# Kernel tuning notes

Hardware: AMD Instinct MI355X
Metric: run time of the kernel (lower is better)

## Reference

```python
import jax, jax.numpy as jnp
import numpy as np

# dims
B, T = 2, 256
E = 512            # n_embd
G = 8              # n_groups
GD = E // G        # group_dim == head_dim == 64
L = 8              # n_layer
N = L * G          # n_nodes == 64
V = 50257          # vocab
S = 8              # n_steps


def _rms(x):
    eps = jnp.asarray(jnp.finfo(x.dtype).eps, x.dtype)
    return x * jax.lax.rsqrt(jnp.mean(x * x, axis=-1, keepdims=True) + eps)


def _rope(x, cos, sin):
    # x: (B,T,N,GD); cos/sin: (T, GD//2)
    d = x.shape[-1] // 2
    x1, x2 = x[..., :d], x[..., d:]
    c = cos[None, :, None, :]
    s = sin[None, :, None, :]
    return jnp.concatenate([x1 * c + x2 * s, -x1 * s + x2 * c], axis=-1)


def setup_inputs() -> dict:
    key = jax.random.key(0)
    ks = jax.random.split(key, 9)
    idx = jax.random.randint(ks[0], (B, T), 0, V, dtype=jnp.int32)
    wte = 0.02 * jax.random.normal(ks[1], (V, E), jnp.float32)
    # adapters: identity block at group slice (per init_weights) + small noise
    ad = np.zeros((N, GD, E), np.float32)
    for i in range(N):
        g = i % G
        ad[i, :, g * GD:(g + 1) * GD] = np.eye(GD, dtype=np.float32)
    adapters = jnp.asarray(ad) + 0.005 * jax.random.normal(ks[2], (N, GD, E), jnp.float32)
    qkv_w = 0.005 * jax.random.normal(ks[3], (N, 3 * GD, GD), jnp.float32)
    attn_proj = 0.005 * jax.random.normal(ks[4], (N, GD, GD), jnp.float32)
    mlp_fc = 0.005 * jax.random.normal(ks[5], (N, 4 * GD, GD), jnp.float32)
    mlp_proj = 0.005 * jax.random.normal(ks[6], (N, GD, 4 * GD), jnp.float32)
    # structured dependency matrix: layer l <- layer l-1, weight 1/G
    D = np.zeros((N, N), np.float32)
    for l in range(1, L):
        D[l * G:(l + 1) * G, (l - 1) * G:l * G] = 1.0 / G
    dep = jnp.asarray(D)
    router_w = (1.0 / np.sqrt(E)) * jax.random.normal(ks[7], (E, 1), jnp.float32)
    router_b = jnp.full((1,), -3.0, jnp.float32)
    lm_head_w = 0.005 * jax.random.normal(ks[8], (V, E), jnp.float32)
    return {"idx": idx, "n_steps": S, "wte": wte, "adapters": adapters,
            "qkv_w": qkv_w, "attn_proj": attn_proj, "mlp_fc": mlp_fc,
            "mlp_proj": mlp_proj, "dep": dep, "router_w": router_w,
            "router_b": router_b, "lm_head_w": lm_head_w}


def _forward(idx, n_steps, wte, adapters, qkv_w, attn_proj, mlp_fc, mlp_proj,
             dep, router_w, router_b, lm_head_w):
    Bs, Ts = idx.shape
    groups = np.arange(N) % G  # static scatter/gather pattern: node -> group slice
    inv_freq = 1.0 / (10000.0 ** (np.arange(0, GD, 2, dtype=np.float64) / GD))
    freqs = np.outer(np.arange(Ts), inv_freq)
    cos = jnp.asarray(np.cos(freqs), jnp.float32)
    sin = jnp.asarray(np.sin(freqs), jnp.float32)

    x = _rms(wte[idx])                                  # (B,T,E)
    p_cont = jnp.ones((Bs, Ts), x.dtype)

    # depths computed under no_grad in torch -> stop_gradient here
    dp = jax.nn.relu(jax.lax.stop_gradient(dep))
    depths = jnp.zeros((N,), x.dtype)
    for _ in range(L):
        depths = dp @ (depths + 1.0)

    causal = np.tril(np.ones((Ts, Ts), bool))
    scale = 1.0 / np.sqrt(GD)

    for t in range(n_steps):
        td = t * (L / n_steps)
        w_all = jnp.exp(-jnp.abs(depths - td))
        # torch gathers active = w_all > 0.15; equivalent dense form: zero-weight inactive
        w_eff = jnp.where(w_all > 0.15, w_all, jnp.zeros_like(w_all))

        xi = (jnp.einsum('bte,nge->btng', x, adapters)
              + x.reshape(Bs, Ts, G, GD)[:, :, groups, :])          # (B,T,N,GD)
        qkv = jnp.einsum('btng,nog->btno', xi, qkv_w).reshape(Bs, Ts, N, 3, GD)
        q, k, v = qkv[..., 0, :], qkv[..., 1, :], qkv[..., 2, :]
        q = _rms(_rope(q, cos, sin))
        k = _rms(_rope(k, cos, sin))
        scores = jnp.einsum('btng,bsng->bnts', q, k) * scale
        scores = jnp.where(causal[None, None], scores, -jnp.inf)
        att = jnp.einsum('bnts,bsng->btng', jax.nn.softmax(scores, axis=-1), v)
        # NOTE: einsum strings below intentionally replicate the original code
        # (k and o are summed out without contraction against the other operand)
        xi_mid = xi + jnp.einsum('btng,ngk->btng', att, attn_proj)
        fc = jnp.einsum('btng,nog->btno', _rms(xi_mid), mlp_fc)
        mp = jnp.einsum('btno,ngk->btng', jnp.square(jax.nn.relu(fc)), mlp_proj)
        up = (xi_mid + mp - xi) * w_eff[None, None, :, None]
        # scatter-add back by group (node n = l*G + g -> group g)
        full_up = up.reshape(Bs, Ts, L, G, GD).sum(axis=2).reshape(Bs, Ts, E)
        x = x + full_up * p_cont[..., None]
        # router (training-mode soft halting; top_fixed=bottom_fixed=0)
        ph = jax.nn.sigmoid(x @ router_w + router_b)[..., 0]
        p_cont = p_cont * (1.0 - ph)

    logits = _rms(x) @ lm_head_w.T
    return 15.0 * jnp.tanh(logits / 15.0)


def reference(idx, n_steps, wte, adapters, qkv_w, attn_proj, mlp_fc, mlp_proj,
              dep, router_w, router_b, lm_head_w):
    return _forward(idx, n_steps, wte, adapters, qkv_w, attn_proj, mlp_fc,
                    mlp_proj, dep, router_w, router_b, lm_head_w)
```

## Files before the change

### kernel.cpp

```cpp
#include <hip/hip_runtime.h>
#include <hip/hip_bf16.h>
#include <math.h>

#define BB 2
#define TT 256
#define BT 512
#define EE 512
#define GG 8
#define GD 64
#define LL 8
#define NN 64
#define VV 50257
#define D2 32
#define EPS 1.1920928955078125e-07f
#define S72 72

typedef __attribute__((ext_vector_type(4))) float floatx4;
typedef __attribute__((ext_vector_type(8))) short short8;

#define OFF_DEPTHS   0
#define OFF_APS      64
#define OFF_MPS      (OFF_APS + NN*GD)
#define OFF_COS      (OFF_MPS + NN*GD)
#define OFF_SIN      (OFF_COS + TT*D2)
#define OFF_X        (OFF_SIN + TT*D2)
#define OFF_PCONT    (OFF_X + BT*EE)
#define OFF_SMLP     (OFF_PCONT + BT)
#define OFF_YBF      (OFF_SMLP + BT*NN)
#define OFF_STEP     (OFF_YBF + (BT*EE)/2)
#define OFF_XI       OFF_STEP
#define OFF_ATT      (OFF_XI + BT*NN*GD)
#define OFF_XBF      (OFF_ATT + BT*NN*GD)
#define OFF_QB       (OFF_XBF + (BT*EE)/2)
#define OFF_KB       (OFF_QB + (BT*NN*GD)/2)
#define OFF_VTB      (OFF_KB + (BT*NN*GD)/2)
#define OFF_ABF      (OFF_VTB + (BT*NN*GD)/2)
#define OFF_QWBF     (OFF_ABF + (NN*GD*EE)/2)
#define OFF_FWBF     (OFF_QWBF + (NN*192*GD)/2)
#define OFF_WBF      OFF_STEP

__device__ __forceinline__ float step_weight(const float* depths, const int* ns, int t, int n) {
    float td = (float)t * (8.0f / (float)ns[0]);
    float wa = expf(-fabsf(depths[n] - td));
    return (wa > 0.15f) ? wa : 0.0f;
}

__global__ void k_prep(const float* __restrict__ dep, float* __restrict__ depths) {
    __shared__ float cur[NN], nxt[NN];
    int i = threadIdx.x;
    if (i < NN) cur[i] = 0.f;
    __syncthreads();
    for (int it = 0; it < LL; ++it) {
        if (i < NN) {
            float acc = 0.f;
            for (int m = 0; m < NN; ++m) acc += fmaxf(dep[i*NN + m], 0.f) * (cur[m] + 1.f);
            nxt[i] = acc;
        }
        __syncthreads();
        if (i < NN) cur[i] = nxt[i];
        __syncthreads();
    }
    if (i < NN) depths[i] = cur[i];
}

__global__ void k_sums(const float* __restrict__ attn_proj, const float* __restrict__ mlp_proj,
                       float* __restrict__ aps, float* __restrict__ mps) {
    int i = blockIdx.x * blockDim.x + threadIdx.x;
    if (i >= NN*GD) return;
    float a = 0.f;
    const float* ap = attn_proj + (size_t)i * GD;
    for (int k = 0; k < GD; ++k) a += ap[k];
    aps[i] = a;
    float m = 0.f;
    const float* mp = mlp_proj + (size_t)i * 4 * GD;
    for (int k = 0; k < 4*GD; ++k) m += mp[k];
    mps[i] = m;
}

__global__ void k_rope_table(float* __restrict__ ctab, float* __restrict__ stab) {
    int i = blockIdx.x * blockDim.x + threadIdx.x;
    if (i >= TT*D2) return;
    int pos = i / D2, f = i % D2;
    double inv = pow(10000.0, -((double)(2*f)) / (double)GD);
    double ang = (double)pos * inv;
    ctab[i] = (float)cos(ang);
    stab[i] = (float)sin(ang);
}

__global__ void k_cvt(const float* __restrict__ src, __hip_bfloat16* __restrict__ dst, int n4) {
    int i = blockIdx.x * blockDim.x + threadIdx.x;
    if (i >= n4) return;
    float4 f = ((const float4*)src)[i];
    __hip_bfloat16 h0 = __float2bfloat16(f.x);
    __hip_bfloat16 h1 = __float2bfloat16(f.y);
    __hip_bfloat16 h2 = __float2bfloat16(f.z);
    __hip_bfloat16 h3 = __float2bfloat16(f.w);
    ushort4 o;
    o.x = *(const unsigned short*)&h0;
    o.y = *(const unsigned short*)&h1;
    o.z = *(const unsigned short*)&h2;
    o.w = *(const unsigned short*)&h3;
    *(ushort4*)(dst + (size_t)i*4) = o;
}

__global__ void k_embed(const int* __restrict__ idx, const float* __restrict__ wte,
                        float* __restrict__ x, __hip_bfloat16* __restrict__ xbf,
                        float* __restrict__ pcont) {
    int bt = blockIdx.x;
    int tid = threadIdx.x;
    const float* src = wte + (size_t)idx[bt] * EE;
    float v0 = src[tid], v1 = src[tid + 256];
    __shared__ float red[4];
    float ss = v0*v0 + v1*v1;
    for (int o = 32; o > 0; o >>= 1) ss += __shfl_xor(ss, o);
    if ((tid & 63) == 0) red[tid >> 6] = ss;
    __syncthreads();
    float sc = rsqrtf((red[0]+red[1]+red[2]+red[3]) / (float)EE + EPS);
    float a = v0 * sc, b = v1 * sc;
    x[bt*EE + tid]       = a;
    x[bt*EE + tid + 256] = b;
    xbf[bt*EE + tid]       = __float2bfloat16(a);
    xbf[bt*EE + tid + 256] = __float2bfloat16(b);
    if (tid == 0) pcont[bt] = 1.f;
}

__global__ __launch_bounds__(256) void k_xi_qkv(const __hip_bfloat16* __restrict__ xbf,
        const __hip_bfloat16* __restrict__ abf, const __hip_bfloat16* __restrict__ qwbf,
        const float* __restrict__ x, float* __restrict__ xi,
        __hip_bfloat16* __restrict__ qb, __hip_bfloat16* __restrict__ kb,
        __hip_bfloat16* __restrict__ vtb,
        const float* __restrict__ ctab, const float* __restrict__ stab,
        const float* __restrict__ depths, const int* __restrict__ ns, int t) {
    int n = blockIdx.y;
    if (step_weight(depths, ns, t, n) == 0.f) return;
    int bt0 = blockIdx.x * 64;
    __shared__ __align__(16) char smem[16640 + 16384 + 9216];
    __hip_bfloat16* sA   = (__hip_bfloat16*)smem;
    float*          obuf = (float*)smem;
    __hip_bfloat16* sB   = (__hip_bfloat16*)(smem + 16640);
    __hip_bfloat16* Bs72 = (__hip_bfloat16*)(smem + 16640);
    __hip_bfloat16* xis  = (__hip_bfloat16*)(smem + 33024);
    int tid = threadIdx.x;
    int wave = tid >> 6, lane = tid & 63;
    int wr = wave >> 1, wc = wave & 1;
    int quad = lane >> 4, l16 = lane & 15;

    size_t goffA[2], goffB[2];
    int sOff[2];
    #pragma unroll
    for (int j = 0; j < 2; ++j) {
        int s = (j*4 + wave)*64 + lane;
        int r = s >> 3;
        int cs = (s & 7) ^ (r & 7);
        goffA[j] = (size_t)(bt0 + r)*EE + cs*8;
        goffB[j] = ((size_t)n*GD + r)*EE + cs*8;
        sOff[j] = (j*4 + wave)*512;
    }

    floatx4 acc[2][2];
    #pragma unroll
    for (int mt = 0; mt < 2; ++mt)
        #pragma unroll
        for (int nt = 0; nt < 2; ++nt) acc[mt][nt] = (floatx4){0.f,0.f,0.f,0.f};

    #pragma unroll
    for (int j = 0; j < 2; ++j) {
        __builtin_amdgcn_global_load_lds(
            (const __attribute__((address_space(1))) void*)(xbf + goffA[j]),
            (__attribute__((address_space(3))) void*)(&sA[sOff[j]]), 16, 0, 0);
        __builtin_amdgcn_global_load_lds(
            (const __attribute__((address_space(1))) void*)(abf + goffB[j]),
            (__attribute__((address_space(3))) void*)(&sB[sOff[j]]), 16, 0, 0);
    }
    __syncthreads();

    int cur = 0;
    #pragma unroll
    for (int kt = 0; kt < 8; ++kt) {
        if (kt < 7) {
            int k0 = (kt + 1) * 64;
            #pragma unroll
            for (int j = 0; j < 2; ++j) {
                __builtin_amdgcn_global_load_lds(
                    (const __attribute__((address_space(1))) void*)(xbf + goffA[j] + k0),
                    (__attribute__((address_space(3))) void*)(&sA[(cur^1)*4096 + sOff[j]]), 16, 0, 0);
                __builtin_amdgcn_global_load_lds(
                    (const __attribute__((address_space(1))) void*)(abf + goffB[j] + k0),
                    (__attribute__((address_space(3))) void*)(&sB[(cur^1)*4096 + sOff[j]]), 16, 0, 0);
            }
        }
        #pragma unroll
        for (int ks = 0; ks < 2; ++ks) {
            short8 af[2], bf[2];
            #pragma unroll
            for (int mt = 0; mt < 2; ++mt) {
                int row = wr*32 + mt*16 + l16;
                int ck = ((ks << 2) | quad) ^ (row & 7);
                af[mt] = *(const short8*)(&sA[cur*4096 + row*64 + ck*8]);
            }
            #pragma unroll
            for (int nt = 0; nt < 2; ++nt) {
                int row = wc*32 + nt*16 + l16;
                int ck = ((ks << 2) | quad) ^ (row & 7);
                bf[nt] = *(const short8*)(&sB[cur*4096 + row*64 + ck*8]);
            }
            #pragma unroll
            for (int mt = 0; mt < 2; ++mt)
                #pragma unroll
                for (int nt = 0; nt < 2; ++nt)
                    acc[mt][nt] = __builtin_amdgcn_mfma_f32_16x16x32_bf16(af[mt], bf[nt], acc[mt][nt], 0, 0, 0);
        }
        __syncthreads();
        cur ^= 1;
    }

    int gofs = (n & (GG-1)) * GD;
    #pragma unroll
    for (int mt = 0; mt < 2; ++mt) {
        #pragma unroll
        for (int nt = 0; nt < 2; ++nt) {
            int col = wc*32 + nt*16 + l16;
            #pragma unroll
            for (int r = 0; r < 4; ++r) {
                int token = wr*32 + mt*16 + quad*4 + r;
                int bt = bt0 + token;
                float val = acc[mt][nt][r] + x[(size_t)bt*EE + gofs + col];
                xi[((size_t)bt*NN + n)*GD + col] = val;
                xis[token*S72 + col] = __float2bfloat16(val);
            }
        }
    }
    __syncthreads();

    const __hip_bfloat16* wbase = qwbf + (size_t)n * 192 * GD;
    int b = bt0 >> 8;
    int t0 = bt0 & (TT - 1);
    for (int c = 0; c < 3; ++c) {
        for (int i = tid; i < 512; i += 256) {
            int r = i >> 3, c8 = (i & 7) * 8;
            *(uint4*)(&Bs72[r*S72 + c8]) = *(const uint4*)(&wbase[(size_t)(c*64 + r)*GD + c8]);
        }
        __syncthreads();
        floatx4 oacc[2][2];
        #pragma unroll
        for (int mt = 0; mt < 2; ++mt)
            #pragma unroll
            for (int nt = 0; nt < 2; ++nt) oacc[mt][nt] = (floatx4){0.f,0.f,0.f,0.f};
        #pragma unroll
        for (int ks = 0; ks < 2; ++ks) {
            short8 af[2], bf[2];
            #pragma unroll
            for (int mt = 0; mt < 2; ++mt)
                af[mt] = *(const short8*)(&xis[(wr*32 + mt*16 + l16)*S72 + ks*32 + quad*8]);
            #pragma unroll
            for (int nt = 0; nt < 2; ++nt)
                bf[nt] = *(const short8*)(&Bs72[(wc*32 + nt*16 + l16)*S72 + ks*32 + quad*8]);
            #pragma unroll
            for (int mt = 0; mt < 2; ++mt)
                #pragma unroll
                for (int nt = 0; nt < 2; ++nt)
                    oacc[mt][nt] = __builtin_amdgcn_mfma_f32_16x16x32_bf16(af[mt], bf[nt], oacc[mt][nt], 0, 0, 0);
        }
        #pragma unroll
        for (int mt = 0; mt < 2; ++mt)
            #pragma unroll
            for (int nt = 0; nt < 2; ++nt)
                #pragma unroll
                for (int r = 0; r < 4; ++r)
                    obuf[(wr*32 + mt*16 + quad*4 + r)*65 + wc*32 + nt*16 + l16] = oacc[mt][nt][r];
        __syncthreads();
        if (c < 2) {
            __hip_bfloat16* dst = (c == 0) ? qb : kb;
            for (int tr = 0; tr < 16; ++tr) {
                int row = wave*16 + tr, bt = bt0 + row;
                float val = obuf[row*65 + lane];
                int pos = bt & (TT - 1);
                float pair = __shfl_xor(val, 32);
                int fi = lane & 31;
                float cc = ctab[pos*D2 + fi], sn = stab[pos*D2 + fi];
                float nv = (lane < 32) ? (val*cc + pair*sn) : (val*cc - pair*sn);
                float ss = nv*nv;
                for (int o = 32; o > 0; o >>= 1) ss += __shfl_xor(ss, o);
                float outv = nv * rsqrtf(ss / (float)GD + EPS);
                dst[((size_t)bt*NN + n)*GD + lane] = __float2bfloat16(outv);
            }
        } else {
            for (int tr = 0; tr < 16; ++tr) {
                int g = wave*16 + tr;
                float vv = obuf[lane*65 + g];
                vtb[(((size_t)(b*NN + n))*GD + g)*TT + t0 + lane] = __float2bfloat16(vv);
            }
        }
        __syncthreads();
    }
}

__global__ __launch_bounds__(256) void k_attn(const __hip_bfloat16* __restrict__ qb,
        const __hip_bfloat16* __restrict__ kb, const __hip_bfloat16* __restrict__ vtb,
        float* __restrict__ att,
        const float* __restrict__ depths, const int* __restrict__ ns, int t) {
    int it = blockIdx.x, b = blockIdx.y, n = blockIdx.z;
    if (step_weight(depths, ns, t, n) == 0.f) return;
    __shared__ __align__(16) __hip_bfloat16 qs[64*S72];
    __shared__ __align__(16) __hip_bfloat16 ksm[64*S72];
    __shared__ __align__(16) __hip_bfloat16 vs[64*S72];
    __shared__ __align__(16) __hip_bfloat16 ps[64*S72];
    int tid = threadIdx.x;
    int wave = tid >> 6, lane = tid & 63;
    int quad = lane >> 4, l16 = lane & 15;
    for (int i = tid; i < 512; i += 256) {
        int r = i >> 3, c8 = (i & 7) * 8;
        *(uint4*)(&qs[r*S72 + c8]) = *(const uint4*)(&qb[(((size_t)(b*TT + it*64 + r))*NN + n)*GD + c8]);
    }
    floatx4 oacc[4];
    float m_i[4], l_i[4];
    #pragma unroll
    for (int nt = 0; nt < 4; ++nt) oacc[nt] = (floatx4){0.f,0.f,0.f,0.f};
    #pragma unroll
    for (int r = 0; r < 4; ++r) { m_i[r] = -INFINITY; l_i[r] = 0.f; }
    __syncthreads();
    for (int ct = 0; ct <= it; ++ct) {
        for (int i = tid; i < 512; i += 256) {
            int r = i >> 3, c8 = (i & 7) * 8;
            *(uint4*)(&ksm[r*S72 + c8]) = *(const uint4*)(&kb[(((size_t)(b*TT + ct*64 + r))*NN + n)*GD + c8]);
            *(uint4*)(&vs[r*S72 + c8])  = *(const uint4*)(&vtb[(((size_t)(b*NN + n))*GD + r)*TT + ct*64 + c8]);
        }
        __syncthreads();
        floatx4 s[4];
        #pragma unroll
        for (int nt = 0; nt < 4; ++nt) s[nt] = (floatx4){0.f,0.f,0.f,0.f};
        #pragma unroll
        for (int ks = 0; ks < 2; ++ks) {
            short8 af = *(const short8*)(&qs[(wave*16 + l16)*S72 + ks*32 + quad*8]);
            #pragma unroll
            for (int nt = 0; nt < 4; ++nt) {
                short8 bf = *(const short8*)(&ksm[(nt*16 + l16)*S72 + ks*32 + quad*8]);
                s[nt] = __builtin_amdgcn_mfma_f32_16x16x32_bf16(af, bf, s[nt], 0, 0, 0);
            }
        }
        #pragma unroll
        for (int r = 0; r < 4; ++r) {
            int rowg = it*64 + wave*16 + quad*4 + r;
            float mx = -INFINITY;
            #pragma unroll
            for (int nt = 0; nt < 4; ++nt) {
                int colg = ct*64 + nt*16 + l16;
                float sv = (colg <= rowg) ? s[nt][r] * 0.125f : -INFINITY;
                s[nt][r] = sv;
                mx = fmaxf(mx, sv);
            }
            for (int o = 8; o > 0; o >>= 1) mx = fmaxf(mx, __shfl_xor(mx, o));
            float mnew = fmaxf(m_i[r], mx);
            float alpha = expf(m_i[r] - mnew);
            float rs = 0.f;
            #pragma unroll
            for (int nt = 0; nt < 4; ++nt) {
                float p = expf(s[nt][r] - mnew);
                s[nt][r] = p;
                rs += p;
            }
            for (int o = 8; o > 0; o >>= 1) rs += __shfl_xor(rs, o);
            l_i[r] = l_i[r]*alpha + rs;
            m_i[r] = mnew;
            #pragma unroll
            for (int nt = 0; nt < 4; ++nt) oacc[nt][r] *= alpha;
        }
        #pragma unroll
        for (int nt = 0; nt < 4; ++nt)
            #pragma unroll
            for (int r = 0; r < 4; ++r)
                ps[(wave*16 + quad*4 + r)*S72 + nt*16 + l16] = __float2bfloat16(s[nt][r]);
        __syncthreads();
        #pragma unroll
        for (int ks = 0; ks < 2; ++ks) {
            short8 af = *(const short8*)(&ps[(wave*16 + l16)*S72 + ks*32 + quad*8]);
            #pragma unroll
            for (int nt = 0; nt < 4; ++nt) {
                short8 bf = *(const short8*)(&vs[(nt*16 + l16)*S72 + ks*32 + quad*8]);
                oacc[nt] = __builtin_amdgcn_mfma_f32_16x16x32_bf16(af, bf, oacc[nt], 0, 0, 0);
            }
        }
        __syncthreads();
    }
    #pragma unroll
    for (int r = 0; r < 4; ++r) {
        float inv = 1.f / l_i[r];
        int token = it*64 + wave*16 + quad*4 + r;
        #pragma unroll
        for (int nt = 0; nt < 4; ++nt)
            att[((size_t)(b*TT + token)*NN + n)*GD + nt*16 + l16] = oacc[nt][r] * inv;
    }
}

__global__ __launch_bounds__(256) void k_fc2(const float* __restrict__ xi, const float* __restrict__ att,
        const float* __restrict__ aps, const __hip_bfloat16* __restrict__ fwbf, float* __restrict__ smlp,
        const float* __restrict__ depths, const int* __restrict__ ns, int t) {
    int n = blockIdx.y;
    if (step_weight(depths, ns, t, n) == 0.f) return;
    int bt0 = blockIdx.x * 64;
    __shared__ __align__(16) __hip_bfloat16 ys[64*S72];
    __shared__ __align__(16) __hip_bfloat16 ws[64*S72];
    __shared__ float sred[64];
    int tid = threadIdx.x;
    int wave = tid >> 6, lane = tid & 63;
    int quad = lane >> 4, l16 = lane & 15;
    for (int tr = 0; tr < 16; ++tr) {
        int row = wave*16 + tr, bt = bt0 + row;
        size_t base = ((size_t)bt*NN + n)*GD + lane;
        float xv = xi[base] + att[base] * aps[n*GD + lane];
        float ss = xv*xv;
        for (int o = 32; o > 0; o >>= 1) ss += __shfl_xor(ss, o);
        ys[row*S72 + lane] = __float2bfloat16(xv * rsqrtf(ss / (float)GD + EPS));
    }
    __syncthreads();
    float rowacc[4] = {0.f, 0.f, 0.f, 0.f};
    for (int c = 0; c < 4; ++c) {
        for (int i = tid; i < 512; i += 256) {
            int r = i >> 3, c8 = (i & 7) * 8;
            *(uint4*)(&ws[r*S72 + c8]) = *(const uint4*)(&fwbf[((size_t)n*256 + c*64 + r)*GD + c8]);
        }
        __syncthreads();
        floatx4 s[4];
        #pragma unroll
        for (int nt = 0; nt < 4; ++nt) s[nt] = (floatx4){0.f,0.f,0.f,0.f};
        #pragma unroll
        for (int ks = 0; ks < 2; ++ks) {
            short8 af = *(const short8*)(&ys[(wave*16 + l16)*S72 + ks*32 + quad*8]);
            #pragma unroll
            for (int nt = 0; nt < 4; ++nt) {
                short8 bf = *(const short8*)(&ws[(nt*16 + l16)*S72 + ks*32 + quad*8]);
                s[nt] = __builtin_amdgcn_mfma_f32_16x16x32_bf16(af, bf, s[nt], 0, 0, 0);
            }
        }
        #pragma unroll
        for (int nt = 0; nt < 4; ++nt)
            #pragma unroll
            for (int r = 0; r < 4; ++r) {
                float rr = fmaxf(s[nt][r], 0.f);
                rowacc[r] += rr*rr;
            }
        __syncthreads();
    }
    #pragma unroll
    for (int r = 0; r < 4; ++r) {
        for (int o = 8; o > 0; o >>= 1) rowacc[r] += __shfl_xor(rowacc[r], o);
        if (l16 == 0) sred[wave*16 + quad*4 + r] = rowacc[r];
    }
    __syncthreads();
    if (tid < 64) smlp[(size_t)(bt0 + tid)*NN + n] = sred[tid];
}

__global__ __launch_bounds__(256) void k_update(float* __restrict__ x, __hip_bfloat16* __restrict__ xbf,
                                                float* __restrict__ pcont,
                                                const float* __restrict__ att, const float* __restrict__ smlp,
                                                const float* __restrict__ aps, const float* __restrict__ mps,
                                                const float* __restrict__ router_w, const float* __restrict__ router_b,
                                                const float* __restrict__ depths, const int* __restrict__ ns, int t,
                                                int last, __hip_bfloat16* __restrict__ ybf) {
    int bt = blockIdx.x, tid = threadIdx.x;
    __shared__ float we[NN];
    __shared__ float red[4];
    __shared__ float red2[4];
    if (tid < NN) we[tid] = step_weight(depths, ns, t, tid);
    __syncthreads();
    float pc = pcont[bt];
    float dot = 0.f, ssq = 0.f;
    float xv0 = 0.f, xv1 = 0.f;
    #pragma unroll
    for (int h = 0; h < 2; ++h) {
        int e = tid + h*256;
        int gq = e >> 6, gd = e & 63;
        float sum = 0.f;
        #pragma unroll
        for (int l = 0; l < LL; ++l) {
            int n = l*GG + gq;
            float w = we[n];
            if (w != 0.f) {
                sum += (att[((size_t)bt*NN + n)*GD + gd] * aps[n*GD + gd]
                        + smlp[bt*NN + n] * mps[n*GD + gd]) * w;
            }
        }
        float xv = x[bt*EE + e] + sum * pc;
        x[bt*EE + e] = xv;
        if (!last) xbf[bt*EE + e] = __float2bfloat16(xv);
        dot += xv * router_w[e];
        ssq += xv * xv;
        if (h == 0) xv0 = xv; else xv1 = xv;
    }
    for (int o = 32; o > 0; o >>= 1) dot += __shfl_xor(dot, o);
    if (last) for (int o = 32; o > 0; o >>= 1) ssq += __shfl_xor(ssq, o);
    if ((tid & 63) == 0) { red[tid >> 6] = dot; red2[tid >> 6] = ssq; }
    __syncthreads();
    if (last) {
        float sc = rsqrtf((red2[0]+red2[1]+red2[2]+red2[3]) / (float)EE + EPS);
        ybf[bt*EE + tid]       = __float2bfloat16(xv0 * sc);
        ybf[bt*EE + tid + 256] = __float2bfloat16(xv1 * sc);
    }
    if (tid == 0) {
        float z = red[0]+red[1]+red[2]+red[3] + router_b[0];
        float ph = 1.f / (1.f + expf(-z));
        pcont[bt] = pc * (1.f - ph);
    }
}

__global__ __launch_bounds__(256) void k_lmhead(const __hip_bfloat16* __restrict__ ybf,
                                                const __hip_bfloat16* __restrict__ wbf,
                                                float* __restrict__ out) {
    int id = blockIdx.x;
    int w = (id & 7) * 200 + (id >> 3);
    int bm = w & 3;
    int bn = w >> 2;
    if (bn >= (VV + 127)/128) return;

    __shared__ __align__(16) __hip_bfloat16 As[2][128*64];
    __shared__ __align__(16) __hip_bfloat16 Bs[2][128*64];
    int tid = threadIdx.x;
    int wave = tid >> 6, lane = tid & 63;
    int wr = wave >> 1, wc = wave & 1;
    int quad = lane >> 4, l16 = lane & 15;

    size_t offA[4], offB[4];
    int ldsOff[4];
    #pragma unroll
    for (int j = 0; j < 4; ++j) {
        int s = (j*4 + wave)*64 + lane;
        int r = s >> 3;
        int cs = (s & 7) ^ (r & 7);
        offA[j] = (size_t)(bm*128 + r)*EE + cs*8;
        int vrow = bn*128 + r; if (vrow >= VV) vrow = VV - 1;
        offB[j] = (size_t)vrow*EE + cs*8;
        ldsOff[j] = (j*4 + wave)*512;
    }

    floatx4 acc[4][4];
    #pragma unroll
    for (int mt = 0; mt < 4; ++mt)
        #pragma unroll
        for (int nt = 0; nt < 4; ++nt)
            acc[mt][nt] = (floatx4){0.f, 0.f, 0.f, 0.f};

    #pragma unroll
    for (int j = 0; j < 4; ++j) {
        __builtin_amdgcn_global_load_lds(
            (const __attribute__((address_space(1))) void*)(ybf + offA[j]),
            (__attribute__((address_space(3))) void*)(&As[0][ldsOff[j]]), 16, 0, 0);
        __builtin_amdgcn_global_load_lds(
            (const __attribute__((address_space(1))) void*)(wbf + offB[j]),
            (__attribute__((address_space(3))) void*)(&Bs[0][ldsOff[j]]), 16, 0, 0);
    }
    __syncthreads();

    int cur = 0;
    for (int kt = 0; kt < 8; ++kt) {
        if (kt < 7) {
            int k0 = (kt + 1) * 64;
            #pragma unroll
            for (int j = 0; j < 4; ++j) {
                __builtin_amdgcn_global_load_lds(
                    (const __attribute__((address_space(1))) void*)(ybf + offA[j] + k0),
                    (__attribute__((address_space(3))) void*)(&As[cur^1][ldsOff[j]]), 16, 0, 0);
                __builtin_amdgcn_global_load_lds(
                    (const __attribute__((address_space(1))) void*)(wbf + offB[j] + k0),
                    (__attribute__((address_space(3))) void*)(&Bs[cur^1][ldsOff[j]]), 16, 0, 0);
            }
        }
        #pragma unroll
        for (int ks = 0; ks < 2; ++ks) {
            short8 af[4], bf[4];
            #pragma unroll
            for (int mt = 0; mt < 4; ++mt) {
                int r = wr*64 + mt*16 + l16;
                int ck = ((ks << 2) | quad) ^ (r & 7);
                af[mt] = *(const short8*)(&As[cur][r*64 + ck*8]);
            }
            #pragma unroll
            for (int nt = 0; nt < 4; ++nt) {
                int r = wc*64 + nt*16 + l16;
                int ck = ((ks << 2) | quad) ^ (r & 7);
                bf[nt] = *(const short8*)(&Bs[cur][r*64 + ck*8]);
            }
            #pragma unroll
            for (int mt = 0; mt < 4; ++mt)
                #pragma unroll
                for (int nt = 0; nt < 4; ++nt)
                    acc[mt][nt] = __builtin_amdgcn_mfma_f32_16x16x32_bf16(af[mt], bf[nt], acc[mt][nt], 0, 0, 0);
        }
        __syncthreads();
        cur ^= 1;
    }

    #pragma unroll
    for (int mt = 0; mt < 4; ++mt) {
        int gm = bm*128 + wr*64 + mt*16 + quad*4;
        #pragma unroll
        for (int nt = 0; nt < 4; ++nt) {
            int gn = bn*128 + wc*64 + nt*16 + l16;
            if (gn < VV) {
                #pragma unroll
                for (int r = 0; r < 4; ++r) {
                    float u = acc[mt][nt][r] * (1.f/15.f);
                    float e = __expf(2.f * u);
                    float th = 1.f - __fdividef(2.f, e + 1.f);
                    out[(size_t)(gm + r)*VV + gn] = 15.f * th;
                }
            }
        }
    }
}

extern "C" void kernel_launch(void* const* d_in, const int* in_sizes, int n_in,
                              void* d_out, int out_size, void* d_ws, size_t ws_size,
                              hipStream_t stream) {
    (void)in_sizes; (void)n_in; (void)out_size; (void)ws_size;
    const int*   idx       = (const int*)d_in[0];
    const int*   nsteps    = (const int*)d_in[1];
    const float* wte       = (const float*)d_in[2];
    const float* adapters  = (const float*)d_in[3];
    const float* qkv_w     = (const float*)d_in[4];
    const float* attn_proj = (const float*)d_in[5];
    const float* mlp_fc    = (const float*)d_in[6];
    const float* mlp_proj  = (const float*)d_in[7];
    const float* dep       = (const float*)d_in[8];
    const float* router_w  = (const float*)d_in[9];
    const float* router_b  = (const float*)d_in[10];
    const float* lm_head   = (const float*)d_in[11];
    float* out = (float*)d_out;
    float* ws  = (float*)d_ws;

    float* depths = ws + OFF_DEPTHS;
    float* aps    = ws + OFF_APS;
    float* mps    = ws + OFF_MPS;
    float* ctab   = ws + OFF_COS;
    float* stab   = ws + OFF_SIN;
    float* x      = ws + OFF_X;
    float* pcont  = ws + OFF_PCONT;
    float* smlp   = ws + OFF_SMLP;
    float* xi     = ws + OFF_XI;
    float* att    = ws + OFF_ATT;
    __hip_bfloat16* xbf  = (__hip_bfloat16*)(ws + OFF_XBF);
    __hip_bfloat16* qb   = (__hip_bfloat16*)(ws + OFF_QB);
    __hip_bfloat16* kb   = (__hip_bfloat16*)(ws + OFF_KB);
    __hip_bfloat16* vtb  = (__hip_bfloat16*)(ws + OFF_VTB);
    __hip_bfloat16* abf  = (__hip_bfloat16*)(ws + OFF_ABF);
    __hip_bfloat16* qwbf = (__hip_bfloat16*)(ws + OFF_QWBF);
    __hip_bfloat16* fwbf = (__hip_bfloat16*)(ws + OFF_FWBF);
    __hip_bfloat16* wbf  = (__hip_bfloat16*)(ws + OFF_WBF);
    __hip_bfloat16* ybf  = (__hip_bfloat16*)(ws + OFF_YBF);

    k_prep<<<1, 64, 0, stream>>>(dep, depths);
    k_sums<<<(NN*GD + 255)/256, 256, 0, stream>>>(attn_proj, mlp_proj, aps, mps);
    k_rope_table<<<(TT*D2 + 255)/256, 256, 0, stream>>>(ctab, stab);
    k_cvt<<<(NN*GD*EE/4 + 255)/256, 256, 0, stream>>>(adapters, abf, NN*GD*EE/4);
    k_cvt<<<(NN*192*GD/4 + 255)/256, 256, 0, stream>>>(qkv_w, qwbf, NN*192*GD/4);
    k_cvt<<<(NN*256*GD/4 + 255)/256, 256, 0, stream>>>(mlp_fc, fwbf, NN*256*GD/4);
    k_embed<<<BT, 256, 0, stream>>>(idx, wte, x, xbf, pcont);

    for (int t = 0; t < 8; ++t) {
        k_xi_qkv<<<dim3(BT/64, NN), 256, 0, stream>>>(xbf, abf, qwbf, x, xi, qb, kb, vtb,
                                                      ctab, stab, depths, nsteps, t);
        k_attn<<<dim3(4, BB, NN), 256, 0, stream>>>(qb, kb, vtb, att, depths, nsteps, t);
        k_fc2<<<dim3(BT/64, NN), 256, 0, stream>>>(xi, att, aps, fwbf, smlp, depths, nsteps, t);
        k_update<<<BT, 256, 0, stream>>>(x, xbf, pcont, att, smlp, aps, mps,
                                         router_w, router_b, depths, nsteps, t,
                                         (t == 7) ? 1 : 0, ybf);
    }

    k_cvt<<<((VV*EE)/4 + 255)/256, 256, 0, stream>>>(lm_head, wbf, (VV*EE)/4);
    k_lmhead<<<1600, 256, 0, stream>>>(ybf, wbf, out);
}
```

Measured before the change: 709.4 us.

## Stage lm_head epilogue through LDS for vectorized stores, single-buffer K loop

The lm_head GEMM epilogue now writes accumulators to shared memory, then has each thread read four consecutive columns and emit a 16-byte packed store of the tanh-capped logits, replacing scattered 4-byte column stores. The target is the large fp32 logits write of about 100 MB. Because the output row stride (V=50257) is odd, rows are only 4-byte aligned, so the code uses a packed struct. To fit the staging buffer, the K loop drops double-buffering and uses one LDS buffer with load-then-sync, which exposes global load latency and adds extra barriers per mt slice.

```diff
diff --git a/kernel.cpp b/kernel.cpp
--- a/kernel.cpp
+++ b/kernel.cpp
@@ -17,6 +17,8 @@
 
 typedef __attribute__((ext_vector_type(4))) float floatx4;
 typedef __attribute__((ext_vector_type(8))) short short8;
+
+struct __attribute__((packed, aligned(4))) f4u { float x, y, z, w; };
 
 #define OFF_DEPTHS   0
 #define OFF_APS      64
@@ -45,6 +47,12 @@
     return (wa > 0.15f) ? wa : 0.0f;
 }
 
+__device__ __forceinline__ float fast_tanh15(float v) {
+    float u = v * (1.f/15.f);
+    float e = __expf(2.f * u);
+    return 15.f * (1.f - __fdividef(2.f, e + 1.f));
+}
+
 __global__ void k_prep(const float* __restrict__ dep, float* __restrict__ depths) {
     __shared__ float cur[NN], nxt[NN];
     int i = threadIdx.x;
@@ -512,8 +520,11 @@
     int bn = w >> 2;
     if (bn >= (VV + 127)/128) return;
 
-    __shared__ __align__(16) __hip_bfloat16 As[2][128*64];
-    __shared__ __align__(16) __hip_bfloat16 Bs[2][128*64];
+    __shared__ __align__(16) char smem[32768];
+    __hip_bfloat16* As  = (__hip_bfloat16*)smem;
+    __hip_bfloat16* Bs  = (__hip_bfloat16*)(smem + 16384);
+    float*          ebuf = (float*)smem;
+
     int tid = threadIdx.x;
     int wave = tid >> 6, lane = tid & 63;
     int wr = wave >> 1, wc = wave & 1;
@@ -539,31 +550,17 @@
         for (int nt = 0; nt < 4; ++nt)
             acc[mt][nt] = (floatx4){0.f, 0.f, 0.f, 0.f};
 
-    #pragma unroll
-    for (int j = 0; j < 4; ++j) {
-        __builtin_amdgcn_global_load_lds(
-            (const __attribute__((address_space(1))) void*)(ybf + offA[j]),
-            (__attribute__((address_space(3))) void*)(&As[0][ldsOff[j]]), 16, 0, 0);
-        __builtin_amdgcn_global_load_lds(
-            (const __attribute__((address_space(1))) void*)(wbf + offB[j]),
-            (__attribute__((address_space(3))) void*)(&Bs[0][ldsOff[j]]), 16, 0, 0);
-    }
-    __syncthreads();
-
-    int cur = 0;
-    for (int kt = 0; kt < 8; ++kt) {
-        if (kt < 7) {
-            int k0 = (kt + 1) * 64;
-            #pragma unroll
-            for (int j = 0; j < 4; ++j) {
-                __builtin_amdgcn_global_load_lds(
-                    (const __attribute__((address_space(1))) void*)(ybf + offA[j] + k0),
-                    (__attribute__((address_space(3))) void*)(&As[cur^1][ldsOff[j]]), 16, 0, 0);
-                __builtin_amdgcn_global_load_lds(
-                    (const __attribute__((address_space(1))) void*)(wbf + offB[j] + k0),
-                    (__attribute__((address_space(3))) void*)(&Bs[cur^1][ldsOff[j]]), 16, 0, 0);
-            }
-        }
+    for (int k0 = 0; k0 < EE; k0 += 64) {
+        #pragma unroll
+        for (int j = 0; j < 4; ++j) {
+            __builtin_amdgcn_global_load_lds(
+                (const __attribute__((address_space(1))) void*)(ybf + offA[j] + k0),
+                (__attribute__((address_space(3))) void*)(&As[ldsOff[j]]), 16, 0, 0);
+            __builtin_amdgcn_global_load_lds(
+                (const __attribute__((address_space(1))) void*)(wbf + offB[j] + k0),
+                (__attribute__((address_space(3))) void*)(&Bs[ldsOff[j]]), 16, 0, 0);
+        }
+        __syncthreads();
         #pragma unroll
         for (int ks = 0; ks < 2; ++ks) {
             short8 af[4], bf[4];
@@ -571,13 +568,13 @@
             for (int mt = 0; mt < 4; ++mt) {
                 int r = wr*64 + mt*16 + l16;
                 int ck = ((ks << 2) | quad) ^ (r & 7);
-                af[mt] = *(const short8*)(&As[cur][r*64 + ck*8]);
+                af[mt] = *(const short8*)(&As[r*64 + ck*8]);
             }
             #pragma unroll
             for (int nt = 0; nt < 4; ++nt) {
                 int r = wc*64 + nt*16 + l16;
                 int ck = ((ks << 2) | quad) ^ (r & 7);
-                bf[nt] = *(const short8*)(&Bs[cur][r*64 + ck*8]);
+                bf[nt] = *(const short8*)(&Bs[r*64 + ck*8]);
             }
             #pragma unroll
             for (int mt = 0; mt < 4; ++mt)
@@ -586,25 +583,40 @@
                     acc[mt][nt] = __builtin_amdgcn_mfma_f32_16x16x32_bf16(af[mt], bf[nt], acc[mt][nt], 0, 0, 0);
         }
         __syncthreads();
-        cur ^= 1;
-    }
-
+    }
+
+    bool lastbn = (bn == (VV >> 7));
     #pragma unroll
     for (int mt = 0; mt < 4; ++mt) {
-        int gm = bm*128 + wr*64 + mt*16 + quad*4;
-        #pragma unroll
-        for (int nt = 0; nt < 4; ++nt) {
-            int gn = bn*128 + wc*64 + nt*16 + l16;
-            if (gn < VV) {
-                #pragma unroll
-                for (int r = 0; r < 4; ++r) {
-                    float u = acc[mt][nt][r] * (1.f/15.f);
-                    float e = __expf(2.f * u);
-                    float th = 1.f - __fdividef(2.f, e + 1.f);
-                    out[(size_t)(gm + r)*VV + gn] = 15.f * th;
-                }
-            }
-        }
+        #pragma unroll
+        for (int nt = 0; nt < 4; ++nt)
+            #pragma unroll
+            for (int r = 0; r < 4; ++r)
+                ebuf[(wr*16 + quad*4 + r)*132 + wc*64 + nt*16 + l16] = acc[mt][nt][r];
+        __syncthreads();
+        #pragma unroll
+        for (int p = 0; p < 4; ++p) {
+            int idx = p*256 + tid;
+            int row = idx >> 5;
+            int col = (idx & 31) * 4;
+            float4 v = *(const float4*)(&ebuf[row*132 + col]);
+            float o0 = fast_tanh15(v.x);
+            float o1 = fast_tanh15(v.y);
+            float o2 = fast_tanh15(v.z);
+            float o3 = fast_tanh15(v.w);
+            int grow = bm*128 + (row >> 4)*64 + mt*16 + (row & 15);
+            int gcol = bn*128 + col;
+            if (!lastbn) {
+                f4u s; s.x = o0; s.y = o1; s.z = o2; s.w = o3;
+                *(f4u*)(&out[(size_t)grow*VV + gcol]) = s;
+            } else {
+                if (gcol + 0 < VV) out[(size_t)grow*VV + gcol + 0] = o0;
+                if (gcol + 1 < VV) out[(size_t)grow*VV + gcol + 1] = o1;
+                if (gcol + 2 < VV) out[(size_t)grow*VV + gcol + 2] = o2;
+                if (gcol + 3 < VV) out[(size_t)grow*VV + gcol + 3] = o3;
+            }
+        }
+        __syncthreads();
     }
 }
 
```

Measured after the change: 714.4 us. About the same (+0.7%).
